# Kernel tuning notes

Measured on AMD Instinct MI355X. Metric: run time of the kernel, lower is better.

Reference implementation:

```python
import jax, jax.numpy as jnp
import numpy as np

N = 50000      # nodes
D = 128        # input_dim == hidden_dim (required by aggrmethod='add')
E_ADJ = 800000 # nonzeros in sparse adjacency
E_PRED = 500000
L = 2          # nbaselayer
BN_EPS = 1e-5


def setup_inputs() -> dict:
    key = jax.random.key(0)
    ks = jax.random.split(key, 10)
    x = jax.random.normal(ks[0], (N, D), dtype=jnp.float32)
    adj_row = jax.random.randint(ks[1], (E_ADJ,), 0, N, dtype=jnp.int32)
    adj_col = jax.random.randint(ks[2], (E_ADJ,), 0, N, dtype=jnp.int32)
    # positive values ~ normalized adjacency weights (avg degree 16)
    adj_val = jax.random.uniform(ks[3], (E_ADJ,), dtype=jnp.float32) / 16.0
    edge_index = jax.random.randint(ks[4], (2, E_PRED), 0, N, dtype=jnp.int32)
    s = 1.0 / np.sqrt(D).astype(np.float32)
    W = jax.random.uniform(ks[5], (L, D, D), jnp.float32, -s, s)
    W_self = jax.random.uniform(ks[6], (L, D, D), jnp.float32, -s, s)
    b = jax.random.uniform(ks[7], (L, D), jnp.float32, -s, s)
    gamma = jnp.ones((L, D), jnp.float32)
    beta = jnp.zeros((L, D), jnp.float32)
    sc = 1.0 / np.sqrt(2 * D).astype(np.float32)
    Wc = jax.random.uniform(ks[8], (2 * D, 1), jnp.float32, -sc, sc)
    bc = jax.random.uniform(ks[9], (1,), jnp.float32, -sc, sc)
    return dict(x=x, adj_row=adj_row, adj_col=adj_col, adj_val=adj_val,
                edge_index=edge_index, W=W, W_self=W_self, b=b,
                gamma=gamma, beta=beta, Wc=Wc, bc=bc)


def _batchnorm(h, g, be):
    # BatchNorm1d over node dim, training-mode (batch) statistics, biased var
    mu = jnp.mean(h, axis=0)
    var = jnp.mean(jnp.square(h - mu), axis=0)
    return g * (h - mu) * jax.lax.rsqrt(var + BN_EPS) + be


def reference(x, adj_row, adj_col, adj_val, edge_index, W, W_self, b, gamma, beta, Wc, bc):
    h = x
    for i in range(L):  # GraphConvolutionBS layers
        support = h @ W[i]                                  # [N, D]
        # spmm(adj, support): gather by col, scale by val, scatter-add by row
        agg = jax.ops.segment_sum(adj_val[:, None] * support[adj_col],
                                  adj_row, num_segments=N)   # [N, D]
        out = agg + h @ W_self[i] + b[i]                    # self-loop + bias
        h = jax.nn.relu(_batchnorm(out, gamma[i], beta[i]))
        # dropout omitted (eval mode)
    node_emb = h + x  # aggrmethod='add', dense=False: residual with block input
    emb1 = node_emb[edge_index[0]]                          # [E_PRED, D]
    emb2 = node_emb[edge_index[1]]
    edge_emb = jnp.concatenate([emb1, emb2], axis=1)        # [E_PRED, 2D]
    return jax.nn.sigmoid(edge_emb @ Wc + bc)               # [E_PRED, 1]
```

## Files before the change

kernel.cpp:

```cpp
#include <hip/hip_runtime.h>
#include <hip/hip_bf16.h>
#include <hip/hip_fp16.h>

#define DD 128
#define BN_EPS 1e-5f
#define SPMM_BLOCKS 2048
#define CAP 64
#define OVF_MAX 4096

typedef __attribute__((ext_vector_type(8))) short bf16x8;
typedef __attribute__((ext_vector_type(4))) float f32x4;

static __device__ __forceinline__ unsigned short f2bf(float f) {
    __hip_bfloat16 h = __float2bfloat16(f);
    return *reinterpret_cast<unsigned short*>(&h);
}
static __device__ __forceinline__ float bf2f(unsigned short u) {
    return __uint_as_float(((unsigned)u) << 16);
}
static __device__ __forceinline__ unsigned pack_rec(int col, float val) {
    __half h = __float2half(val);
    unsigned hb = *reinterpret_cast<unsigned short*>(&h);
    return (unsigned)col | (hb << 16);
}
static __device__ __forceinline__ float rec_val(unsigned rec) {
    unsigned short hb = (unsigned short)(rec >> 16);
    __half h = *reinterpret_cast<__half*>(&hb);
    return __half2float(h);
}

__global__ __launch_bounds__(256) void prep_zero(
    const float* __restrict__ W, const float* __restrict__ Wself,
    unsigned short* __restrict__ Wt4, int* __restrict__ zp, int nz)
{
    if (blockIdx.x < 32) {
        int mat   = blockIdx.x >> 3;
        int chunk = blockIdx.x & 7;
        int layer = mat >> 1;
        const float* src = (mat & 1) ? (Wself + layer * 16384) : (W + layer * 16384);
        unsigned short* dst = Wt4 + (size_t)mat * 16384;
        int base = chunk * 2048 + threadIdx.x * 4;
        #pragma unroll
        for (int rep = 0; rep < 2; rep++) {
            int i = base + rep * 1024;
            float4 v = *(const float4*)&src[i];
            int k = i >> 7, n = i & 127;
            dst[(n + 0) * 128 + k] = f2bf(v.x);
            dst[(n + 1) * 128 + k] = f2bf(v.y);
            dst[(n + 2) * 128 + k] = f2bf(v.z);
            dst[(n + 3) * 128 + k] = f2bf(v.w);
        }
    } else {
        int i = (blockIdx.x - 32) * 256 + threadIdx.x;
        if (i < nz) zp[i] = 0;
    }
}

__global__ __launch_bounds__(1024) void scatter_bucket(
    const int* __restrict__ arow, const int* __restrict__ acol,
    const float* __restrict__ aval, int* __restrict__ cnt,
    unsigned* __restrict__ bucket, int* __restrict__ ovfc,
    int2* __restrict__ ovf, int E, int rpp)
{
    const int p     = blockIdx.x & 7;
    const int slice = blockIdx.x >> 3;
    const int nsl   = gridDim.x >> 3;
    const int e0    = (int)((long long)E * slice / nsl);
    const int e1    = (int)((long long)E * (slice + 1) / nsl);
    for (int e = e0 + threadIdx.x; e < e1; e += 1024) {
        int r = arow[e];
        if (r / rpp == p) {
            int pos = atomicAdd(&cnt[r], 1);
            unsigned rec = pack_rec(acol[e], aval[e]);
            if (pos < CAP) {
                __builtin_nontemporal_store(rec, &bucket[(size_t)r * CAP + pos]);
            } else {
                int oi = atomicAdd(ovfc, 1);
                if (oi < OVF_MAX) ovf[oi] = make_int2(r, (int)rec);
            }
        }
    }
}

__global__ __launch_bounds__(256) void gemm_mfma(
    const float* __restrict__ A,
    const unsigned short* __restrict__ Wt, const unsigned short* __restrict__ Wst,
    const float* __restrict__ bias,
    const float* __restrict__ stats, const float* __restrict__ gamma,
    const float* __restrict__ beta, float invN, int useBN,
    unsigned short* __restrict__ support, float* __restrict__ outb, int N)
{
    __shared__ float ssc[128], ssh[128];
    if (useBN) {
        if (threadIdx.x < 128) {
            int c = threadIdx.x;
            float mean = stats[c] * invN;
            float var  = stats[128 + c] * invN - mean * mean;
            float sc   = gamma[c] * rsqrtf(var + BN_EPS);
            ssc[c] = sc;
            ssh[c] = beta[c] - mean * sc;
        }
        __syncthreads();
    }

    const int wave = threadIdx.x >> 6;
    const int lane = threadIdx.x & 63;
    const int m    = lane & 15;
    const int quad = lane >> 4;
    const int row0 = blockIdx.x * 64 + wave * 16;

    int arow = row0 + m; if (arow > N - 1) arow = N - 1;
    const float* Ar = A + (size_t)arow * 128;
    bf16x8 af[4];
    #pragma unroll
    for (int ch = 0; ch < 4; ch++) {
        int k0 = ch * 32 + quad * 8;
        float4 u = *(const float4*)&Ar[k0];
        float4 v = *(const float4*)&Ar[k0 + 4];
        float vals[8] = {u.x, u.y, u.z, u.w, v.x, v.y, v.z, v.w};
        #pragma unroll
        for (int j = 0; j < 8; j++) {
            float val = vals[j];
            if (useBN) {
                val = val * ssc[k0 + j] + ssh[k0 + j];
                val = val > 0.f ? val : 0.f;
            }
            af[ch][j] = (short)f2bf(val);
        }
    }

    f32x4 acc1[8], acc2[8];
    #pragma unroll
    for (int nt = 0; nt < 8; nt++) {
        acc1[nt] = (f32x4)(0.f);
        acc2[nt] = (f32x4)(0.f);
    }

    #pragma unroll
    for (int nt = 0; nt < 8; nt++) {
        const bf16x8* B1 = (const bf16x8*)(Wt  + ((size_t)(nt * 16 + m)) * 128 + quad * 8);
        const bf16x8* B2 = (const bf16x8*)(Wst + ((size_t)(nt * 16 + m)) * 128 + quad * 8);
        acc1[nt] = __builtin_amdgcn_mfma_f32_16x16x32_bf16(af[0], B1[0],  acc1[nt], 0, 0, 0);
        acc2[nt] = __builtin_amdgcn_mfma_f32_16x16x32_bf16(af[0], B2[0],  acc2[nt], 0, 0, 0);
        acc1[nt] = __builtin_amdgcn_mfma_f32_16x16x32_bf16(af[1], B1[4],  acc1[nt], 0, 0, 0);
        acc2[nt] = __builtin_amdgcn_mfma_f32_16x16x32_bf16(af[1], B2[4],  acc2[nt], 0, 0, 0);
        acc1[nt] = __builtin_amdgcn_mfma_f32_16x16x32_bf16(af[2], B1[8],  acc1[nt], 0, 0, 0);
        acc2[nt] = __builtin_amdgcn_mfma_f32_16x16x32_bf16(af[2], B2[8],  acc2[nt], 0, 0, 0);
        acc1[nt] = __builtin_amdgcn_mfma_f32_16x16x32_bf16(af[3], B1[12], acc1[nt], 0, 0, 0);
        acc2[nt] = __builtin_amdgcn_mfma_f32_16x16x32_bf16(af[3], B2[12], acc2[nt], 0, 0, 0);
    }

    float bv[8];
    #pragma unroll
    for (int nt = 0; nt < 8; nt++) bv[nt] = bias[nt * 16 + m];

    #pragma unroll
    for (int r = 0; r < 4; r++) {
        int orow = row0 + quad * 4 + r;
        if (orow < N) {
            size_t base = (size_t)orow * 128 + m;
            #pragma unroll
            for (int nt = 0; nt < 8; nt++) {
                support[base + nt * 16] = f2bf(acc1[nt][r]);
                outb[base + nt * 16]    = acc2[nt][r] + bv[nt];
            }
        }
    }
}

__global__ __launch_bounds__(256) void spmm_stats(
    const int* __restrict__ cnt, const unsigned* __restrict__ bucket,
    const int* __restrict__ ovfc, const int2* __restrict__ ovf,
    const unsigned short* __restrict__ sup, float* __restrict__ outb,
    float* __restrict__ partials, int ngroups, int N)
{
    const int r    = threadIdx.x & 31;
    const int slot = threadIdx.x >> 5;
    float s4[4] = {0.f, 0.f, 0.f, 0.f};
    float q4[4] = {0.f, 0.f, 0.f, 0.f};

    for (int g = blockIdx.x; g < ngroups; g += gridDim.x) {
        int row = g * 8 + slot;
        if (row >= N) continue;
        int nrec = cnt[row]; if (nrec > CAP) nrec = CAP;
        const unsigned* packed = bucket + (size_t)row * CAP;

        float4 acc = make_float4(0.f, 0.f, 0.f, 0.f);
        int e = 0;
        for (; e + 4 <= nrec; e += 4) {
            unsigned p0 = packed[e + 0];
            unsigned p1 = packed[e + 1];
            unsigned p2 = packed[e + 2];
            unsigned p3 = packed[e + 3];
            ushort4 s0 = *(const ushort4*)&sup[((size_t)(p0 & 0xFFFFu) << 7) + r * 4];
            ushort4 s1 = *(const ushort4*)&sup[((size_t)(p1 & 0xFFFFu) << 7) + r * 4];
            ushort4 s2 = *(const ushort4*)&sup[((size_t)(p2 & 0xFFFFu) << 7) + r * 4];
            ushort4 s3 = *(const ushort4*)&sup[((size_t)(p3 & 0xFFFFu) << 7) + r * 4];
            float v0 = rec_val(p0), v1 = rec_val(p1);
            float v2 = rec_val(p2), v3 = rec_val(p3);
            acc.x += v0 * bf2f(s0.x); acc.y += v0 * bf2f(s0.y);
            acc.z += v0 * bf2f(s0.z); acc.w += v0 * bf2f(s0.w);
            acc.x += v1 * bf2f(s1.x); acc.y += v1 * bf2f(s1.y);
            acc.z += v1 * bf2f(s1.z); acc.w += v1 * bf2f(s1.w);
            acc.x += v2 * bf2f(s2.x); acc.y += v2 * bf2f(s2.y);
            acc.z += v2 * bf2f(s2.z); acc.w += v2 * bf2f(s2.w);
            acc.x += v3 * bf2f(s3.x); acc.y += v3 * bf2f(s3.y);
            acc.z += v3 * bf2f(s3.z); acc.w += v3 * bf2f(s3.w);
        }
        for (; e < nrec; e++) {
            unsigned pr = packed[e];
            ushort4 sv = *(const ushort4*)&sup[((size_t)(pr & 0xFFFFu) << 7) + r * 4];
            float v = rec_val(pr);
            acc.x += v * bf2f(sv.x); acc.y += v * bf2f(sv.y);
            acc.z += v * bf2f(sv.z); acc.w += v * bf2f(sv.w);
        }

        int oc = *ovfc;
        if (oc > 0) {
            if (oc > OVF_MAX) oc = OVF_MAX;
            for (int i = 0; i < oc; i++) {
                int2 orec = ovf[i];
                if (orec.x == row) {
                    unsigned pr = (unsigned)orec.y;
                    ushort4 sv = *(const ushort4*)&sup[((size_t)(pr & 0xFFFFu) << 7) + r * 4];
                    float v = rec_val(pr);
                    acc.x += v * bf2f(sv.x); acc.y += v * bf2f(sv.y);
                    acc.z += v * bf2f(sv.z); acc.w += v * bf2f(sv.w);
                }
            }
        }

        float4* op = (float4*)&outb[((size_t)row << 7) + r * 4];
        float4 o = *op;
        o.x += acc.x; o.y += acc.y; o.z += acc.z; o.w += acc.w;
        *op = o;
        s4[0] += o.x; s4[1] += o.y; s4[2] += o.z; s4[3] += o.w;
        q4[0] += o.x * o.x; q4[1] += o.y * o.y; q4[2] += o.z * o.z; q4[3] += o.w * o.w;
    }

    __shared__ float red[8][128];
    #pragma unroll
    for (int j = 0; j < 4; j++) red[slot][r * 4 + j] = s4[j];
    __syncthreads();
    float ts = 0.f;
    if (threadIdx.x < 128) {
        #pragma unroll
        for (int j = 0; j < 8; j++) ts += red[j][threadIdx.x];
        partials[(size_t)blockIdx.x * 256 + threadIdx.x] = ts;
    }
    __syncthreads();
    #pragma unroll
    for (int j = 0; j < 4; j++) red[slot][r * 4 + j] = q4[j];
    __syncthreads();
    if (threadIdx.x < 128) {
        float tq = 0.f;
        #pragma unroll
        for (int j = 0; j < 8; j++) tq += red[j][threadIdx.x];
        partials[(size_t)blockIdx.x * 256 + 128 + threadIdx.x] = tq;
    }
}

__global__ __launch_bounds__(256) void reduce_stats(
    const float* __restrict__ partials, float* __restrict__ stats, int nblk)
{
    int g = blockIdx.x;
    int per = (nblk + gridDim.x - 1) / gridDim.x;
    int b0 = g * per, b1 = min(b0 + per, nblk);
    float a0 = 0.f;
    for (int b = b0; b < b1; b++) {
        a0 += partials[(size_t)b * 256 + threadIdx.x];
    }
    atomicAdd(&stats[threadIdx.x], a0);
}

__global__ __launch_bounds__(256) void score_kernel(
    const float* __restrict__ outb, const float* __restrict__ stats,
    const float* __restrict__ gamma, const float* __restrict__ beta,
    const float* __restrict__ x, const float* __restrict__ Wc,
    float* __restrict__ s1, float* __restrict__ s2, float invN, int N)
{
    int idx = blockIdx.x * 256 + threadIdx.x;
    if (idx >= N * 32) return;
    int c4 = (idx & 31) * 4;
    float4 o = *(const float4*)&outb[(size_t)idx * 4];
    float res[4];
    const float* op = &o.x;
    #pragma unroll
    for (int j = 0; j < 4; j++) {
        int c = c4 + j;
        float mean = stats[c] * invN;
        float var  = stats[128 + c] * invN - mean * mean;
        float sc   = gamma[c] * rsqrtf(var + BN_EPS);
        float sh   = beta[c] - mean * sc;
        float v    = op[j] * sc + sh;
        res[j] = v > 0.f ? v : 0.f;
    }
    float4 xv = *(const float4*)&x[(size_t)idx * 4];
    res[0] += xv.x; res[1] += xv.y; res[2] += xv.z; res[3] += xv.w;
    float4 w1 = *(const float4*)&Wc[c4];
    float4 w2 = *(const float4*)&Wc[128 + c4];
    float a1 = res[0] * w1.x + res[1] * w1.y + res[2] * w1.z + res[3] * w1.w;
    float a2 = res[0] * w2.x + res[1] * w2.y + res[2] * w2.z + res[3] * w2.w;
    #pragma unroll
    for (int off = 1; off < 32; off <<= 1) {
        a1 += __shfl_xor(a1, off);
        a2 += __shfl_xor(a2, off);
    }
    if ((idx & 31) == 0) {
        int row = idx >> 5;
        s1[row] = a1;
        s2[row] = a2;
    }
}

__global__ __launch_bounds__(256) void edge_pred_scalar(
    const float* __restrict__ s1, const float* __restrict__ s2,
    const int* __restrict__ ei, const float* __restrict__ bc,
    float* __restrict__ outp, int Ep)
{
    int e = blockIdx.x * 256 + threadIdx.x;
    if (e >= Ep) return;
    float v = s1[ei[e]] + s2[ei[Ep + e]] + bc[0];
    outp[e] = 1.f / (1.f + expf(-v));
}

extern "C" void kernel_launch(void* const* d_in, const int* in_sizes, int n_in,
                              void* d_out, int out_size, void* d_ws, size_t ws_size,
                              hipStream_t stream) {
    const float* x        = (const float*)d_in[0];
    const int*   adj_row  = (const int*)  d_in[1];
    const int*   adj_col  = (const int*)  d_in[2];
    const float* adj_val  = (const float*)d_in[3];
    const int*   ei       = (const int*)  d_in[4];
    const float* W        = (const float*)d_in[5];
    const float* W_self   = (const float*)d_in[6];
    const float* b        = (const float*)d_in[7];
    const float* gamma    = (const float*)d_in[8];
    const float* beta     = (const float*)d_in[9];
    const float* Wc       = (const float*)d_in[10];
    const float* bc       = (const float*)d_in[11];
    float* outp = (float*)d_out;

    const int N  = in_sizes[0] / DD;
    const int E  = in_sizes[1];
    const int Ep = in_sizes[4] / 2;
    const float invN = 1.f / (float)N;

    size_t nd = (size_t)N * DD;
    char* p = (char*)d_ws;
    unsigned short* support16 = (unsigned short*)p; p += nd * 2;
    float*          outbA     = (float*)p;          p += nd * 4;
    float*          outbB     = (float*)p;          p += nd * 4;
    unsigned short* Wt4       = (unsigned short*)p; p += 4 * 16384 * 2;
    float*          stats     = (float*)p;          p += 512 * 4;
    int*            cnt       = (int*)p;            p += (size_t)N * 4;
    int*            ovfc      = (int*)p;            p += 4;
    unsigned*       bucket    = (unsigned*)p;       p += (size_t)N * CAP * 4;
    int2*           ovf       = (int2*)p;           p += (size_t)OVF_MAX * 8;
    float*          s1        = (float*)p;          p += (size_t)N * 4;
    float*          s2        = (float*)p;          p += (size_t)N * 4;
    float*          partials  = (float*)p;          p += (size_t)SPMM_BLOCKS * 256 * 4;

    const int rpp = (N + 7) / 8;
    const int ngroups = (N + 7) / 8;
    const int nz = 512 + N + 1;

    prep_zero<<<32 + (nz + 255) / 256, 256, 0, stream>>>(W, W_self, Wt4, (int*)stats, nz);
    scatter_bucket<<<256, 1024, 0, stream>>>(
        adj_row, adj_col, adj_val, cnt, bucket, ovfc, ovf, E, rpp);

    const int gemm_grid  = (N + 63) / 64;
    const int score_grid = (N * 32 + 255) / 256;

    gemm_mfma<<<gemm_grid, 256, 0, stream>>>(
        x, Wt4 + 0 * 16384, Wt4 + 1 * 16384, b,
        nullptr, nullptr, nullptr, invN, 0,
        support16, outbA, N);
    spmm_stats<<<SPMM_BLOCKS, 256, 0, stream>>>(
        cnt, bucket, ovfc, ovf, support16, outbA, partials, ngroups, N);
    reduce_stats<<<32, 256, 0, stream>>>(partials, stats, SPMM_BLOCKS);

    gemm_mfma<<<gemm_grid, 256, 0, stream>>>(
        outbA, Wt4 + 2 * 16384, Wt4 + 3 * 16384, b + DD,
        stats, gamma, beta, invN, 1,
        support16, outbB, N);
    spmm_stats<<<SPMM_BLOCKS, 256, 0, stream>>>(
        cnt, bucket, ovfc, ovf, support16, outbB, partials, ngroups, N);
    reduce_stats<<<32, 256, 0, stream>>>(partials, stats + 256, SPMM_BLOCKS);

    score_kernel<<<score_grid, 256, 0, stream>>>(
        outbB, stats + 256, gamma + DD, beta + DD, x, Wc, s1, s2, invN, N);
    edge_pred_scalar<<<(Ep + 255) / 256, 256, 0, stream>>>(s1, s2, ei, bc, outp, Ep);
}
```

Baseline: 332.8 us.

## Fuse layer-0 GEMM with edge bucketing and fold stats reduction into consumers

Runs the layer-0 MFMA GEMM and the edge bucketing scatter in one launch, with block halves split between the two tasks. It replaces the separate reduce_stats launches with atomic accumulation into 64 slot buffers; the next GEMM and the score kernel sum those slots themselves. It also lowers the bucket capacity from 64 to 32 (spilling more edges to a larger overflow list), drops the nontemporal store, reorders the GEMM epilogue to cut accumulator registers, and makes the score kernel grid-strided. The aim is fewer launches and less bucket memory traffic, at the cost of more overflow handling, atomic contention and redundant per-block slot reductions.

New measurement: 389.6 us. +17.1%, slower.

```diff
diff --git a/kernel.cpp b/kernel.cpp
--- a/kernel.cpp
+++ b/kernel.cpp
@@ -5,8 +5,10 @@
 #define DD 128
 #define BN_EPS 1e-5f
 #define SPMM_BLOCKS 2048
-#define CAP 64
-#define OVF_MAX 4096
+#define FUSE_GRID 2048
+#define NSLOT 64
+#define CAP 32
+#define OVF_MAX 8192
 
 typedef __attribute__((ext_vector_type(8))) short bf16x8;
 typedef __attribute__((ext_vector_type(4))) float f32x4;
@@ -29,51 +31,42 @@
     return __half2float(h);
 }
 
-__global__ __launch_bounds__(256) void prep_zero(
-    const float* __restrict__ W, const float* __restrict__ Wself,
-    unsigned short* __restrict__ Wt4, int* __restrict__ zp, int nz)
-{
-    if (blockIdx.x < 32) {
-        int mat   = blockIdx.x >> 3;
-        int chunk = blockIdx.x & 7;
-        int layer = mat >> 1;
-        const float* src = (mat & 1) ? (Wself + layer * 16384) : (W + layer * 16384);
-        unsigned short* dst = Wt4 + (size_t)mat * 16384;
-        int base = chunk * 2048 + threadIdx.x * 4;
-        #pragma unroll
-        for (int rep = 0; rep < 2; rep++) {
-            int i = base + rep * 1024;
-            float4 v = *(const float4*)&src[i];
-            int k = i >> 7, n = i & 127;
-            dst[(n + 0) * 128 + k] = f2bf(v.x);
-            dst[(n + 1) * 128 + k] = f2bf(v.y);
-            dst[(n + 2) * 128 + k] = f2bf(v.z);
-            dst[(n + 3) * 128 + k] = f2bf(v.w);
-        }
-    } else {
-        int i = (blockIdx.x - 32) * 256 + threadIdx.x;
-        if (i < nz) zp[i] = 0;
-    }
-}
-
-__global__ __launch_bounds__(1024) void scatter_bucket(
+static __device__ __forceinline__ void dev_prep_w(
+    int mat, int chunk, const float* __restrict__ W,
+    const float* __restrict__ Wself, unsigned short* __restrict__ Wt4)
+{
+    int layer = mat >> 1;
+    const float* src = (mat & 1) ? (Wself + layer * 16384) : (W + layer * 16384);
+    unsigned short* dst = Wt4 + (size_t)mat * 16384;
+    int base = chunk * 2048 + threadIdx.x * 4;
+    #pragma unroll
+    for (int rep = 0; rep < 2; rep++) {
+        int i = base + rep * 1024;
+        float4 v = *(const float4*)&src[i];
+        int k = i >> 7, n = i & 127;
+        dst[(n + 0) * 128 + k] = f2bf(v.x);
+        dst[(n + 1) * 128 + k] = f2bf(v.y);
+        dst[(n + 2) * 128 + k] = f2bf(v.z);
+        dst[(n + 3) * 128 + k] = f2bf(v.w);
+    }
+}
+
+static __device__ __forceinline__ void dev_scatter(
+    int slice, int nsl, int p,
     const int* __restrict__ arow, const int* __restrict__ acol,
     const float* __restrict__ aval, int* __restrict__ cnt,
     unsigned* __restrict__ bucket, int* __restrict__ ovfc,
     int2* __restrict__ ovf, int E, int rpp)
 {
-    const int p     = blockIdx.x & 7;
-    const int slice = blockIdx.x >> 3;
-    const int nsl   = gridDim.x >> 3;
-    const int e0    = (int)((long long)E * slice / nsl);
-    const int e1    = (int)((long long)E * (slice + 1) / nsl);
-    for (int e = e0 + threadIdx.x; e < e1; e += 1024) {
+    const int e0 = (int)((long long)E * slice / nsl);
+    const int e1 = (int)((long long)E * (slice + 1) / nsl);
+    for (int e = e0 + threadIdx.x; e < e1; e += 256) {
         int r = arow[e];
         if (r / rpp == p) {
             int pos = atomicAdd(&cnt[r], 1);
             unsigned rec = pack_rec(acol[e], aval[e]);
             if (pos < CAP) {
-                __builtin_nontemporal_store(rec, &bucket[(size_t)r * CAP + pos]);
+                bucket[(size_t)r * CAP + pos] = rec;
             } else {
                 int oi = atomicAdd(ovfc, 1);
                 if (oi < OVF_MAX) ovf[oi] = make_int2(r, (int)rec);
@@ -82,35 +75,20 @@
     }
 }
 
-__global__ __launch_bounds__(256) void gemm_mfma(
-    const float* __restrict__ A,
+static __device__ __forceinline__ void dev_gemm_tile(
+    int t, const float* __restrict__ A,
     const unsigned short* __restrict__ Wt, const unsigned short* __restrict__ Wst,
-    const float* __restrict__ bias,
-    const float* __restrict__ stats, const float* __restrict__ gamma,
-    const float* __restrict__ beta, float invN, int useBN,
+    const float* __restrict__ bias, const float* ssc, const float* ssh, int useBN,
     unsigned short* __restrict__ support, float* __restrict__ outb, int N)
 {
-    __shared__ float ssc[128], ssh[128];
-    if (useBN) {
-        if (threadIdx.x < 128) {
-            int c = threadIdx.x;
-            float mean = stats[c] * invN;
-            float var  = stats[128 + c] * invN - mean * mean;
-            float sc   = gamma[c] * rsqrtf(var + BN_EPS);
-            ssc[c] = sc;
-            ssh[c] = beta[c] - mean * sc;
-        }
-        __syncthreads();
-    }
-
     const int wave = threadIdx.x >> 6;
     const int lane = threadIdx.x & 63;
     const int m    = lane & 15;
     const int quad = lane >> 4;
-    const int row0 = blockIdx.x * 64 + wave * 16;
-
-    int arow = row0 + m; if (arow > N - 1) arow = N - 1;
-    const float* Ar = A + (size_t)arow * 128;
+    const int row0 = t * 64 + wave * 16;
+
+    int ar = row0 + m; if (ar > N - 1) ar = N - 1;
+    const float* Ar = A + (size_t)ar * 128;
     bf16x8 af[4];
     #pragma unroll
     for (int ch = 0; ch < 4; ch++) {
@@ -129,46 +107,65 @@
         }
     }
 
-    f32x4 acc1[8], acc2[8];
-    #pragma unroll
-    for (int nt = 0; nt < 8; nt++) {
-        acc1[nt] = (f32x4)(0.f);
-        acc2[nt] = (f32x4)(0.f);
-    }
-
     #pragma unroll
     for (int nt = 0; nt < 8; nt++) {
         const bf16x8* B1 = (const bf16x8*)(Wt  + ((size_t)(nt * 16 + m)) * 128 + quad * 8);
         const bf16x8* B2 = (const bf16x8*)(Wst + ((size_t)(nt * 16 + m)) * 128 + quad * 8);
-        acc1[nt] = __builtin_amdgcn_mfma_f32_16x16x32_bf16(af[0], B1[0],  acc1[nt], 0, 0, 0);
-        acc2[nt] = __builtin_amdgcn_mfma_f32_16x16x32_bf16(af[0], B2[0],  acc2[nt], 0, 0, 0);
-        acc1[nt] = __builtin_amdgcn_mfma_f32_16x16x32_bf16(af[1], B1[4],  acc1[nt], 0, 0, 0);
-        acc2[nt] = __builtin_amdgcn_mfma_f32_16x16x32_bf16(af[1], B2[4],  acc2[nt], 0, 0, 0);
-        acc1[nt] = __builtin_amdgcn_mfma_f32_16x16x32_bf16(af[2], B1[8],  acc1[nt], 0, 0, 0);
-        acc2[nt] = __builtin_amdgcn_mfma_f32_16x16x32_bf16(af[2], B2[8],  acc2[nt], 0, 0, 0);
-        acc1[nt] = __builtin_amdgcn_mfma_f32_16x16x32_bf16(af[3], B1[12], acc1[nt], 0, 0, 0);
-        acc2[nt] = __builtin_amdgcn_mfma_f32_16x16x32_bf16(af[3], B2[12], acc2[nt], 0, 0, 0);
-    }
-
-    float bv[8];
-    #pragma unroll
-    for (int nt = 0; nt < 8; nt++) bv[nt] = bias[nt * 16 + m];
-
-    #pragma unroll
-    for (int r = 0; r < 4; r++) {
-        int orow = row0 + quad * 4 + r;
-        if (orow < N) {
-            size_t base = (size_t)orow * 128 + m;
-            #pragma unroll
-            for (int nt = 0; nt < 8; nt++) {
-                support[base + nt * 16] = f2bf(acc1[nt][r]);
-                outb[base + nt * 16]    = acc2[nt][r] + bv[nt];
+        f32x4 a1 = (f32x4)(0.f), a2 = (f32x4)(0.f);
+        a1 = __builtin_amdgcn_mfma_f32_16x16x32_bf16(af[0], B1[0],  a1, 0, 0, 0);
+        a2 = __builtin_amdgcn_mfma_f32_16x16x32_bf16(af[0], B2[0],  a2, 0, 0, 0);
+        a1 = __builtin_amdgcn_mfma_f32_16x16x32_bf16(af[1], B1[4],  a1, 0, 0, 0);
+        a2 = __builtin_amdgcn_mfma_f32_16x16x32_bf16(af[1], B2[4],  a2, 0, 0, 0);
+        a1 = __builtin_amdgcn_mfma_f32_16x16x32_bf16(af[2], B1[8],  a1, 0, 0, 0);
+        a2 = __builtin_amdgcn_mfma_f32_16x16x32_bf16(af[2], B2[8],  a2, 0, 0, 0);
+        a1 = __builtin_amdgcn_mfma_f32_16x16x32_bf16(af[3], B1[12], a1, 0, 0, 0);
+        a2 = __builtin_amdgcn_mfma_f32_16x16x32_bf16(af[3], B2[12], a2, 0, 0, 0);
+        float bvn = bias[nt * 16 + m];
+        #pragma unroll
+        for (int r = 0; r < 4; r++) {
+            int orow = row0 + quad * 4 + r;
+            if (orow < N) {
+                size_t base = (size_t)orow * 128 + m + nt * 16;
+                support[base] = f2bf(a1[r]);
+                outb[base]    = a2[r] + bvn;
             }
         }
     }
 }
 
-__global__ __launch_bounds__(256) void spmm_stats(
+__global__ __launch_bounds__(256) void prep_zero_k(
+    const float* __restrict__ W, const float* __restrict__ Wself,
+    unsigned short* __restrict__ Wt4, int* __restrict__ zp, int nz)
+{
+    if (blockIdx.x < 32) {
+        dev_prep_w(blockIdx.x >> 3, blockIdx.x & 7, W, Wself, Wt4);
+    } else {
+        int i = (blockIdx.x - 32) * 256 + threadIdx.x;
+        if (i < nz) zp[i] = 0;
+    }
+}
+
+__global__ __launch_bounds__(256) void gemm_l0_scatter_k(
+    const float* __restrict__ A,
+    const unsigned short* __restrict__ Wt, const unsigned short* __restrict__ Wst,
+    const float* __restrict__ bias,
+    unsigned short* __restrict__ support, float* __restrict__ outb, int N, int gemm_tiles,
+    const int* __restrict__ arow, const int* __restrict__ acol,
+    const float* __restrict__ aval, int* __restrict__ cnt,
+    unsigned* __restrict__ bucket, int* __restrict__ ovfc,
+    int2* __restrict__ ovf, int E, int rpp)
+{
+    if (((blockIdx.x >> 3) & 1) == 0) {
+        dev_scatter(blockIdx.x >> 4, FUSE_GRID >> 4, blockIdx.x & 7,
+                    arow, acol, aval, cnt, bucket, ovfc, ovf, E, rpp);
+    } else {
+        for (int t = (blockIdx.x >> 4) * 8 + (blockIdx.x & 7); t < gemm_tiles;
+             t += (FUSE_GRID >> 1))
+            dev_gemm_tile(t, A, Wt, Wst, bias, nullptr, nullptr, 0, support, outb, N);
+    }
+}
+
+__global__ __launch_bounds__(256) void spmm_stats_k(
     const int* __restrict__ cnt, const unsigned* __restrict__ bucket,
     const int* __restrict__ ovfc, const int2* __restrict__ ovf,
     const unsigned short* __restrict__ sup, float* __restrict__ outb,
@@ -178,6 +175,7 @@
     const int slot = threadIdx.x >> 5;
     float s4[4] = {0.f, 0.f, 0.f, 0.f};
     float q4[4] = {0.f, 0.f, 0.f, 0.f};
+    __shared__ float red[8][128];
 
     for (int g = blockIdx.x; g < ngroups; g += gridDim.x) {
         int row = g * 8 + slot;
@@ -238,7 +236,6 @@
         q4[0] += o.x * o.x; q4[1] += o.y * o.y; q4[2] += o.z * o.z; q4[3] += o.w * o.w;
     }
 
-    __shared__ float red[8][128];
     #pragma unroll
     for (int j = 0; j < 4; j++) red[slot][r * 4 + j] = s4[j];
     __syncthreads();
@@ -246,7 +243,6 @@
     if (threadIdx.x < 128) {
         #pragma unroll
         for (int j = 0; j < 8; j++) ts += red[j][threadIdx.x];
-        partials[(size_t)blockIdx.x * 256 + threadIdx.x] = ts;
     }
     __syncthreads();
     #pragma unroll
@@ -256,64 +252,100 @@
         float tq = 0.f;
         #pragma unroll
         for (int j = 0; j < 8; j++) tq += red[j][threadIdx.x];
-        partials[(size_t)blockIdx.x * 256 + 128 + threadIdx.x] = tq;
-    }
-}
-
-__global__ __launch_bounds__(256) void reduce_stats(
-    const float* __restrict__ partials, float* __restrict__ stats, int nblk)
-{
-    int g = blockIdx.x;
-    int per = (nblk + gridDim.x - 1) / gridDim.x;
-    int b0 = g * per, b1 = min(b0 + per, nblk);
-    float a0 = 0.f;
-    for (int b = b0; b < b1; b++) {
-        a0 += partials[(size_t)b * 256 + threadIdx.x];
-    }
-    atomicAdd(&stats[threadIdx.x], a0);
-}
-
-__global__ __launch_bounds__(256) void score_kernel(
-    const float* __restrict__ outb, const float* __restrict__ stats,
+        float* slotp = partials + (size_t)(blockIdx.x & (NSLOT - 1)) * 256;
+        atomicAdd(&slotp[threadIdx.x], ts);
+        atomicAdd(&slotp[128 + threadIdx.x], tq);
+    }
+}
+
+__global__ __launch_bounds__(256) void gemm_bn_k(
+    const float* __restrict__ A,
+    const unsigned short* __restrict__ Wt, const unsigned short* __restrict__ Wst,
+    const float* __restrict__ bias,
+    const float* __restrict__ partials, const float* __restrict__ gamma,
+    const float* __restrict__ beta, float invN,
+    unsigned short* __restrict__ support, float* __restrict__ outb, int N)
+{
+    __shared__ float tot[256];
+    __shared__ float sa[128], sb[128];
+    {
+        float a = 0.f;
+        #pragma unroll 8
+        for (int s = 0; s < NSLOT; s++)
+            a += partials[(size_t)s * 256 + threadIdx.x];
+        tot[threadIdx.x] = a;
+    }
+    __syncthreads();
+    if (threadIdx.x < 128) {
+        int c = threadIdx.x;
+        float mean = tot[c] * invN;
+        float var  = tot[128 + c] * invN - mean * mean;
+        float sc   = gamma[c] * rsqrtf(var + BN_EPS);
+        sa[c] = sc;
+        sb[c] = beta[c] - mean * sc;
+    }
+    __syncthreads();
+    dev_gemm_tile(blockIdx.x, A, Wt, Wst, bias, sa, sb, 1, support, outb, N);
+}
+
+__global__ __launch_bounds__(256) void score_k(
+    const float* __restrict__ outb, const float* __restrict__ partials,
     const float* __restrict__ gamma, const float* __restrict__ beta,
     const float* __restrict__ x, const float* __restrict__ Wc,
     float* __restrict__ s1, float* __restrict__ s2, float invN, int N)
 {
-    int idx = blockIdx.x * 256 + threadIdx.x;
-    if (idx >= N * 32) return;
-    int c4 = (idx & 31) * 4;
-    float4 o = *(const float4*)&outb[(size_t)idx * 4];
-    float res[4];
-    const float* op = &o.x;
-    #pragma unroll
-    for (int j = 0; j < 4; j++) {
-        int c = c4 + j;
-        float mean = stats[c] * invN;
-        float var  = stats[128 + c] * invN - mean * mean;
+    __shared__ float tot[256];
+    __shared__ float sa[128], sb[128];
+    {
+        float a = 0.f;
+        #pragma unroll 8
+        for (int s = 0; s < NSLOT; s++)
+            a += partials[(size_t)s * 256 + threadIdx.x];
+        tot[threadIdx.x] = a;
+    }
+    __syncthreads();
+    if (threadIdx.x < 128) {
+        int c = threadIdx.x;
+        float mean = tot[c] * invN;
+        float var  = tot[128 + c] * invN - mean * mean;
         float sc   = gamma[c] * rsqrtf(var + BN_EPS);
-        float sh   = beta[c] - mean * sc;
-        float v    = op[j] * sc + sh;
-        res[j] = v > 0.f ? v : 0.f;
-    }
-    float4 xv = *(const float4*)&x[(size_t)idx * 4];
-    res[0] += xv.x; res[1] += xv.y; res[2] += xv.z; res[3] += xv.w;
-    float4 w1 = *(const float4*)&Wc[c4];
-    float4 w2 = *(const float4*)&Wc[128 + c4];
-    float a1 = res[0] * w1.x + res[1] * w1.y + res[2] * w1.z + res[3] * w1.w;
-    float a2 = res[0] * w2.x + res[1] * w2.y + res[2] * w2.z + res[3] * w2.w;
-    #pragma unroll
-    for (int off = 1; off < 32; off <<= 1) {
-        a1 += __shfl_xor(a1, off);
-        a2 += __shfl_xor(a2, off);
-    }
-    if ((idx & 31) == 0) {
-        int row = idx >> 5;
-        s1[row] = a1;
-        s2[row] = a2;
-    }
-}
-
-__global__ __launch_bounds__(256) void edge_pred_scalar(
+        sa[c] = sc;
+        sb[c] = beta[c] - mean * sc;
+    }
+    __syncthreads();
+
+    int total = N * 32;
+    int stride = gridDim.x * 256;
+    for (int idx = blockIdx.x * 256 + threadIdx.x; idx < total; idx += stride) {
+        int c4 = (idx & 31) * 4;
+        float4 o = *(const float4*)&outb[(size_t)idx * 4];
+        float res[4];
+        const float* op = &o.x;
+        #pragma unroll
+        for (int j = 0; j < 4; j++) {
+            float v = op[j] * sa[c4 + j] + sb[c4 + j];
+            res[j] = v > 0.f ? v : 0.f;
+        }
+        float4 xv = *(const float4*)&x[(size_t)idx * 4];
+        res[0] += xv.x; res[1] += xv.y; res[2] += xv.z; res[3] += xv.w;
+        float4 w1 = *(const float4*)&Wc[c4];
+        float4 w2 = *(const float4*)&Wc[128 + c4];
+        float a1 = res[0] * w1.x + res[1] * w1.y + res[2] * w1.z + res[3] * w1.w;
+        float a2 = res[0] * w2.x + res[1] * w2.y + res[2] * w2.z + res[3] * w2.w;
+        #pragma unroll
+        for (int off = 1; off < 32; off <<= 1) {
+            a1 += __shfl_xor(a1, off);
+            a2 += __shfl_xor(a2, off);
+        }
+        if ((idx & 31) == 0) {
+            int row = idx >> 5;
+            s1[row] = a1;
+            s2[row] = a2;
+        }
+    }
+}
+
+__global__ __launch_bounds__(256) void edge_pred_k(
     const float* __restrict__ s1, const float* __restrict__ s2,
     const int* __restrict__ ei, const float* __restrict__ bc,
     float* __restrict__ outp, int Ep)
@@ -341,10 +373,10 @@
     const float* bc       = (const float*)d_in[11];
     float* outp = (float*)d_out;
 
-    const int N  = in_sizes[0] / DD;
-    const int E  = in_sizes[1];
-    const int Ep = in_sizes[4] / 2;
-    const float invN = 1.f / (float)N;
+    int N  = in_sizes[0] / DD;
+    int E  = in_sizes[1];
+    int Ep = in_sizes[4] / 2;
+    float invN = 1.f / (float)N;
 
     size_t nd = (size_t)N * DD;
     char* p = (char*)d_ws;
@@ -352,43 +384,36 @@
     float*          outbA     = (float*)p;          p += nd * 4;
     float*          outbB     = (float*)p;          p += nd * 4;
     unsigned short* Wt4       = (unsigned short*)p; p += 4 * 16384 * 2;
-    float*          stats     = (float*)p;          p += 512 * 4;
+    float*          partialsA = (float*)p;          p += (size_t)NSLOT * 256 * 4;
+    float*          partialsB = (float*)p;          p += (size_t)NSLOT * 256 * 4;
     int*            cnt       = (int*)p;            p += (size_t)N * 4;
     int*            ovfc      = (int*)p;            p += 4;
     unsigned*       bucket    = (unsigned*)p;       p += (size_t)N * CAP * 4;
     int2*           ovf       = (int2*)p;           p += (size_t)OVF_MAX * 8;
     float*          s1        = (float*)p;          p += (size_t)N * 4;
-    float*          s2        = (float*)p;          p += (size_t)N * 4;
-    float*          partials  = (float*)p;          p += (size_t)SPMM_BLOCKS * 256 * 4;
-
-    const int rpp = (N + 7) / 8;
-    const int ngroups = (N + 7) / 8;
-    const int nz = 512 + N + 1;
-
-    prep_zero<<<32 + (nz + 255) / 256, 256, 0, stream>>>(W, W_self, Wt4, (int*)stats, nz);
-    scatter_bucket<<<256, 1024, 0, stream>>>(
+    float*          s2        = (float*)p;
+
+    int gemm_tiles = (N + 63) / 64;
+    int ngroups    = (N + 7) / 8;
+    int rpp        = (N + 7) / 8;
+    int nz         = NSLOT * 256 * 2 + N + 1;
+
+    prep_zero_k<<<32 + (nz + 255) / 256, 256, 0, stream>>>(
+        W, W_self, Wt4, (int*)partialsA, nz);
+
+    gemm_l0_scatter_k<<<FUSE_GRID, 256, 0, stream>>>(
+        x, Wt4, Wt4 + 16384, b, support16, outbA, N, gemm_tiles,
         adj_row, adj_col, adj_val, cnt, bucket, ovfc, ovf, E, rpp);
-
-    const int gemm_grid  = (N + 63) / 64;
-    const int score_grid = (N * 32 + 255) / 256;
-
-    gemm_mfma<<<gemm_grid, 256, 0, stream>>>(
-        x, Wt4 + 0 * 16384, Wt4 + 1 * 16384, b,
-        nullptr, nullptr, nullptr, invN, 0,
-        support16, outbA, N);
-    spmm_stats<<<SPMM_BLOCKS, 256, 0, stream>>>(
-        cnt, bucket, ovfc, ovf, support16, outbA, partials, ngroups, N);
-    reduce_stats<<<32, 256, 0, stream>>>(partials, stats, SPMM_BLOCKS);
-
-    gemm_mfma<<<gemm_grid, 256, 0, stream>>>(
+    spmm_stats_k<<<SPMM_BLOCKS, 256, 0, stream>>>(
+        cnt, bucket, ovfc, ovf, support16, outbA, partialsA, ngroups, N);
+
+    gemm_bn_k<<<gemm_tiles, 256, 0, stream>>>(
         outbA, Wt4 + 2 * 16384, Wt4 + 3 * 16384, b + DD,
-        stats, gamma, beta, invN, 1,
-        support16, outbB, N);
-    spmm_stats<<<SPMM_BLOCKS, 256, 0, stream>>>(
-        cnt, bucket, ovfc, ovf, support16, outbB, partials, ngroups, N);
-    reduce_stats<<<32, 256, 0, stream>>>(partials, stats + 256, SPMM_BLOCKS);
-
-    score_kernel<<<score_grid, 256, 0, stream>>>(
-        outbB, stats + 256, gamma + DD, beta + DD, x, Wc, s1, s2, invN, N);
-    edge_pred_scalar<<<(Ep + 255) / 256, 256, 0, stream>>>(s1, s2, ei, bc, outp, Ep);
-}
+        partialsA, gamma, beta, invN, support16, outbB, N);
+    spmm_stats_k<<<SPMM_BLOCKS, 256, 0, stream>>>(
+        cnt, bucket, ovfc, ovf, support16, outbB, partialsB, ngroups, N);
+
+    score_k<<<2048, 256, 0, stream>>>(
+        outbB, partialsB, gamma + DD, beta + DD, x, Wc, s1, s2, invN, N);
+    edge_pred_k<<<(Ep + 255) / 256, 256, 0, stream>>>(s1, s2, ei, bc, outp, Ep);
+}
```
